# Kernel tuning notes

Measured on AMD Instinct MI355X. Metric: run time of the kernel, lower is better.

The kernel has to match this reference:

```python
import jax, jax.numpy as jnp
import numpy as np

N = 100000
E = 1600000
F_IN, HID, N_CLS = 128, 16, 32


def setup_inputs() -> dict:
    key = jax.random.key(0)
    ks = jax.random.split(key, 10)
    x = jax.random.normal(ks[0], (N, F_IN), dtype=jnp.float32)
    edge_index = jax.random.randint(ks[1], (2, E), 0, N, dtype=jnp.int64)
    edge_weight = jax.random.uniform(ks[2], (E,), dtype=jnp.float32)
    def glorot(k, shape):
        lim = np.sqrt(6.0 / (shape[0] + shape[1])).astype(np.float32)
        return jax.random.uniform(k, shape, dtype=jnp.float32, minval=-lim, maxval=lim)
    return {
        'x': x, 'edge_index': edge_index, 'edge_weight': edge_weight,
        'W1_0': glorot(ks[3], (F_IN, HID)), 'W1_1': glorot(ks[4], (F_IN, HID)),
        'b1': jnp.zeros((HID,), jnp.float32),
        'W2_0': glorot(ks[5], (HID, N_CLS)), 'W2_1': glorot(ks[6], (HID, N_CLS)),
        'b2': jnp.zeros((N_CLS,), jnp.float32),
    }


def _cheb_conv_k2(x, row, col, edge_weight, W0, W1, b):
    # PyG ChebConv, K=2, lambda_max=2.0:
    #   T0 = x; T1 = L_hat x = D^{-1/2} A D^{-1/2} x - x
    n = x.shape[0]
    deg = jax.ops.segment_sum(edge_weight, row, num_segments=n)  # [N]
    dinv = jnp.where(deg > 0, jax.lax.rsqrt(deg), 0.0)
    norm = dinv[row] * edge_weight * dinv[col]                   # [E]
    agg = jax.ops.segment_sum(norm[:, None] * x[col], row, num_segments=n)  # [N,F]
    tx1 = agg - x
    return x @ W0 + tx1 @ W1 + b


def reference(x, edge_index, edge_weight, W1_0, W1_1, b1, W2_0, W2_1, b2):
    row, col = edge_index[0], edge_index[1]
    h = jax.nn.relu(_cheb_conv_k2(x, row, col, edge_weight, W1_0, W1_1, b1))
    # dropout(p=0) and DFA layers are identity in forward
    out = _cheb_conv_k2(h, row, col, edge_weight, W2_0, W2_1, b2)
    return jax.nn.log_softmax(out, axis=1)
```

## Files before the change

### kernel.cpp

```cpp
#include <hip/hip_runtime.h>
#include <hip/hip_bf16.h>


#include <hip/hip_fp16.h>

constexpr int NN   = 100000;
constexpr int NE   = 1600000;
constexpr int FIN  = 128;
constexpr int HID  = 16;
constexpr int NCLS = 32;

constexpr int RB    = 256;
constexpr int NBKT  = (NN + RB - 1) / RB;
constexpr int EPB   = 4096;
constexpr int EPT   = EPB / 256;
constexpr int GP    = (NE + EPB - 1) / EPB;
constexpr int NTOT  = NBKT * GP;
constexpr int SCAN_CHUNK = 512;
constexpr int NBS   = (NTOT + SCAN_CHUNK - 1) / SCAN_CHUNK;
constexpr int CAP   = 8192;

typedef float f32x2 __attribute__((ext_vector_type(2)));

#if defined(__has_builtin)
#if __has_builtin(__builtin_amdgcn_cvt_pk_f32_fp8)
#define HAVE_CVT_FP8 1
#endif
#endif

static __device__ __forceinline__ unsigned int f2e4m3(float f) {
    union { float f; unsigned int u; } v; v.f = f;
    unsigned int s = (v.u >> 24) & 0x80u;
    unsigned int au = v.u & 0x7fffffffu;
    if (au > 0x43E00000u) au = 0x43E00000u;
    au += 0x7ffffu + ((au >> 20) & 1u);
    int e4 = (int)(au >> 23) - 120;
    unsigned int m = (au >> 20) & 7u;
    unsigned int byte = (e4 <= 0) ? 0u : (((unsigned int)e4 << 3) | m);
    return s | byte;
}
static __device__ __forceinline__ void fp8x4_fma(unsigned int v, float w, float* acc) {
#ifdef HAVE_CVT_FP8
    f32x2 lo = __builtin_amdgcn_cvt_pk_f32_fp8((int)v, false);
    f32x2 hi = __builtin_amdgcn_cvt_pk_f32_fp8((int)v, true);
    acc[0] += w * lo.x; acc[1] += w * lo.y;
    acc[2] += w * hi.x; acc[3] += w * hi.y;
#else
#pragma unroll
    for (int i = 0; i < 4; i++) {
        unsigned int b = (v >> (8 * i)) & 0xffu;
        float f = __int_as_float((int)(((b & 0x80u) << 24) | ((b & 0x7fu) << 20))) * 0x1p120f;
        acc[i] += w * f;
    }
#endif
}
static __device__ __forceinline__ unsigned int wpack(float wf) {
    unsigned int b = __float_as_uint(wf) + 0x8000u;
    return (b >> 16) & 0x7fffu;
}
static __device__ __forceinline__ float wdec(unsigned int u) {
    return __uint_as_float((u >> 17) << 16);
}

__global__ __launch_bounds__(256) void k_hist(const int* __restrict__ row,
                                              int* __restrict__ blockhist) {
    __shared__ int hist[NBKT];
    int tid = threadIdx.x;
    for (int i = tid; i < NBKT; i += 256) hist[i] = 0;
    __syncthreads();
    long ebase = (long)blockIdx.x * EPB;
#pragma unroll
    for (int i = 0; i < EPT; i++) {
        long e = ebase + i * 256 + tid;
        if (e < NE) atomicAdd(&hist[row[e] >> 8], 1);
    }
    __syncthreads();
    for (int i = tid; i < NBKT; i += 256)
        blockhist[i * GP + blockIdx.x] = hist[i];
}

__global__ __launch_bounds__(SCAN_CHUNK) void k_scan_block(
    const int* __restrict__ in, int* __restrict__ outExcl,
    int* __restrict__ bsum, int n) {
    __shared__ int sh[SCAN_CHUNK];
    int tid = threadIdx.x;
    int i = blockIdx.x * SCAN_CHUNK + tid;
    int v = (i < n) ? in[i] : 0;
    sh[tid] = v;
    __syncthreads();
    for (int off = 1; off < SCAN_CHUNK; off <<= 1) {
        int t = (tid >= off) ? sh[tid - off] : 0;
        __syncthreads();
        sh[tid] += t;
        __syncthreads();
    }
    if (i < n) outExcl[i] = sh[tid] - v;
    if (tid == SCAN_CHUNK - 1) bsum[blockIdx.x] = sh[tid];
}

__global__ void k_scan_tops(int* __restrict__ bsum, int nb) {
    int lane = threadIdx.x;
    int v[8], e[8];
    int s = 0;
#pragma unroll
    for (int t = 0; t < 8; t++) {
        int idx = lane * 8 + t;
        v[t] = (idx < nb) ? bsum[idx] : 0;
        e[t] = s;
        s += v[t];
    }
    int sc = s;
    for (int off = 1; off < 64; off <<= 1) {
        int up = __shfl_up(sc, off, 64);
        if (lane >= off) sc += up;
    }
    int excl = sc - s;
#pragma unroll
    for (int t = 0; t < 8; t++) {
        int idx = lane * 8 + t;
        if (idx < nb) bsum[idx] = excl + e[t];
    }
}

__global__ void k_scan_add(int* __restrict__ outExcl, const int* __restrict__ bsum, int n) {
    int i = blockIdx.x * blockDim.x + threadIdx.x;
    if (i < n) outExcl[i] += bsum[i >> 9];
}

__global__ __launch_bounds__(256) void k_partition(
    const int* __restrict__ row, const int* __restrict__ col,
    const float* __restrict__ w, const int* __restrict__ scanExcl,
    int2* __restrict__ part) {
    __shared__ int2 stage[EPB];
    __shared__ unsigned short sbkt[EPB];
    __shared__ int cnt[NBKT];
    __shared__ int lofs[NBKT];
    __shared__ int cursor[NBKT];
    __shared__ int gbase[NBKT];
    __shared__ int sa[512], sb[512];
    int tid = threadIdx.x;
    long ebase = (long)blockIdx.x * EPB;
    int rr[EPT]; int cc[EPT]; float wv[EPT];
#pragma unroll
    for (int i = 0; i < EPT; i++) {
        long e = ebase + i * 256 + tid;
        if (e < NE) { rr[i] = row[e]; cc[i] = col[e]; wv[i] = w[e]; }
        else rr[i] = -1;
    }
    for (int i = tid; i < NBKT; i += 256) cnt[i] = 0;
    __syncthreads();
#pragma unroll
    for (int i = 0; i < EPT; i++)
        if (rr[i] >= 0) atomicAdd(&cnt[rr[i] >> 8], 1);
    __syncthreads();
    for (int i = tid; i < 512; i += 256) sa[i] = (i < NBKT) ? cnt[i] : 0;
    __syncthreads();
    int* src = sa; int* dst = sb;
    for (int off = 1; off < 512; off <<= 1) {
        for (int i = tid; i < 512; i += 256)
            dst[i] = src[i] + ((i >= off) ? src[i - off] : 0);
        __syncthreads();
        int* t = src; src = dst; dst = t;
    }
    for (int i = tid; i < NBKT; i += 256) {
        int ex = src[i] - cnt[i];
        lofs[i] = ex;
        cursor[i] = ex;
        gbase[i] = scanExcl[i * GP + blockIdx.x];
    }
    __syncthreads();
#pragma unroll
    for (int i = 0; i < EPT; i++) {
        if (rr[i] >= 0) {
            int b = rr[i] >> 8;
            int p = atomicAdd(&cursor[b], 1);
            int2 v;
            v.x = cc[i] | ((rr[i] & 255) << 17);
            v.y = __float_as_int(wv[i]);
            stage[p] = v;
            sbkt[p] = (unsigned short)b;
        }
    }
    __syncthreads();
    int total = (int)min((long)EPB, NE - ebase);
    for (int i = tid; i < total; i += 256) {
        int b = sbkt[i];
        part[gbase[b] + (i - lofs[b])] = stage[i];
    }
}

__global__ __launch_bounds__(256) void k_bucket_sort(
    const int2* __restrict__ part, const int* __restrict__ scanExcl,
    unsigned int* __restrict__ partC, int* __restrict__ rowptr,
    float* __restrict__ dinv) {
    __shared__ int2 stage[CAP];
    __shared__ int hist[RB];
    __shared__ int cursor[RB];
    __shared__ int wtot[4];
    int b = blockIdx.x;
    int tid = threadIdx.x;
    int start = scanExcl[b * GP];
    int end = (b + 1 < NBKT) ? scanExcl[(b + 1) * GP] : NE;
    int count = end - start;
    hist[tid] = 0;
    __syncthreads();
    for (int i = tid; i < count; i += 256)
        atomicAdd(&hist[(part[start + i].x >> 17) & 255], 1);
    __syncthreads();
    int lane = tid & 63, wv = tid >> 6;
    int v = hist[tid];
    int sc = v;
#pragma unroll
    for (int off = 1; off < 64; off <<= 1) {
        int up = __shfl_up(sc, off, 64);
        if (lane >= off) sc += up;
    }
    if (lane == 63) wtot[wv] = sc;
    __syncthreads();
    int add = 0;
    for (int w2 = 0; w2 < wv; w2++) add += wtot[w2];
    int ex = sc + add - v;
    int node = b * RB + tid;
    if (node <= NN) rowptr[node] = start + ex;
    cursor[tid] = ex;
    __syncthreads();
    for (int i = tid; i < count; i += 256) {
        int2 p = part[start + i];
        int rl = (p.x >> 17) & 255;
        int pos = atomicAdd(&cursor[rl], 1);
        int2 c; c.x = p.x & 0x1FFFF; c.y = p.y;
        if (pos < CAP) stage[pos] = c;
    }
    __syncthreads();
    {
        int rend = cursor[tid];
        float d = 0.f;
        for (int i = ex; i < rend; i++) d += __int_as_float(stage[i].y);
        if (node < NN) dinv[node] = d > 0.f ? rsqrtf(d) : 0.f;
    }
    for (int i = tid; i < count; i += 256)
        if (i < CAP) {
            int2 p = stage[i];
            partC[start + i] = (unsigned int)p.x | (wpack(__int_as_float(p.y)) << 17);
        }
}

__global__ __launch_bounds__(256) void k_proj1(
    const float* __restrict__ x, const float* __restrict__ W0,
    const float* __restrict__ W1, const float* __restrict__ b1,
    const float* __restrict__ dinv,
    float* __restrict__ xa, unsigned char* __restrict__ xb8) {
    long t = (long)blockIdx.x * 256 + threadIdx.x;
    bool valid = t < NN;
    long n = valid ? t : 0;
    const float4* xg = (const float4*)x + n * 32;
    float accA[HID], accB[HID];
#pragma unroll
    for (int o = 0; o < HID; o++) { accA[o] = 0.f; accB[o] = 0.f; }
    float4 bufA[8], bufB[8];
#pragma unroll
    for (int m = 0; m < 8; m++) bufA[m] = xg[m];
#pragma unroll
    for (int m = 0; m < 8; m++) bufB[m] = xg[8 + m];

#define PROJ1_CHUNK(BUF, C)                                            \
    {                                                                   \
        const float* W0p = W0 + (C) * 32 * HID;                         \
        const float* W1p = W1 + (C) * 32 * HID;                         \
        _Pragma("unroll")                                               \
        for (int m = 0; m < 8; m++) {                                   \
            float xv[4] = {BUF[m].x, BUF[m].y, BUF[m].z, BUF[m].w};     \
            _Pragma("unroll")                                           \
            for (int q = 0; q < 4; q++) {                               \
                int k = m * 4 + q;                                      \
                _Pragma("unroll")                                       \
                for (int o = 0; o < HID; o++) accA[o] += xv[q] * W0p[k * HID + o]; \
                _Pragma("unroll")                                       \
                for (int o = 0; o < HID; o++) accB[o] += xv[q] * W1p[k * HID + o]; \
            }                                                           \
        }                                                               \
    }

    PROJ1_CHUNK(bufA, 0)
#pragma unroll
    for (int m = 0; m < 8; m++) bufA[m] = xg[16 + m];
    PROJ1_CHUNK(bufB, 1)
#pragma unroll
    for (int m = 0; m < 8; m++) bufB[m] = xg[24 + m];
    PROJ1_CHUNK(bufA, 2)
    PROJ1_CHUNK(bufB, 3)
#undef PROJ1_CHUNK

    if (!valid) return;
    float4* xap = (float4*)(xa + n * HID);
#pragma unroll
    for (int q = 0; q < 4; q++) {
        float4 va;
        va.x = accA[4*q+0] - accB[4*q+0] + b1[4*q+0];
        va.y = accA[4*q+1] - accB[4*q+1] + b1[4*q+1];
        va.z = accA[4*q+2] - accB[4*q+2] + b1[4*q+2];
        va.w = accA[4*q+3] - accB[4*q+3] + b1[4*q+3];
        xap[q] = va;
    }
    float dn = dinv[n];
    unsigned int pk[4];
#pragma unroll
    for (int q = 0; q < 4; q++)
        pk[q] = f2e4m3(dn * accB[4*q+0]) | (f2e4m3(dn * accB[4*q+1]) << 8)
              | (f2e4m3(dn * accB[4*q+2]) << 16) | (f2e4m3(dn * accB[4*q+3]) << 24);
    *(uint4*)(xb8 + n * HID) = make_uint4(pk[0], pk[1], pk[2], pk[3]);
}

__global__ __launch_bounds__(256) void k_gather1(
    const int* __restrict__ rowptr, const unsigned int* __restrict__ partC,
    const float* __restrict__ dinv, const unsigned char* __restrict__ xb8,
    float* __restrict__ agg1) {
    long t = (long)blockIdx.x * 256 + threadIdx.x;
    int n = (int)(t >> 6);
    if (n >= NN) return;
    int lane = threadIdx.x & 63;
    int d = lane & 3, p = lane >> 2;
    int s = rowptr[n], e = rowptr[n + 1];
    float acc[4] = {0.f, 0.f, 0.f, 0.f};
    for (int j = s + p; j < e; j += 16) {
        unsigned int u = partC[j];
        unsigned int v = *(const unsigned int*)(xb8 + (u & 0x1FFFF) * HID + d * 4);
        fp8x4_fma(v, wdec(u), acc);
    }
#pragma unroll
    for (int i = 0; i < 4; i++) {
        acc[i] += __shfl_xor(acc[i], 4);
        acc[i] += __shfl_xor(acc[i], 8);
        acc[i] += __shfl_xor(acc[i], 16);
        acc[i] += __shfl_xor(acc[i], 32);
    }
    if (p == 0) {
        float dn = dinv[n];
        float4 o; o.x = dn * acc[0]; o.y = dn * acc[1];
        o.z = dn * acc[2]; o.w = dn * acc[3];
        *(float4*)(agg1 + (long)n * HID + d * 4) = o;
    }
}

__global__ __launch_bounds__(256) void k_proj2(
    const float* __restrict__ xa, const float* __restrict__ agg1,
    const float* __restrict__ W0, const float* __restrict__ W1,
    const float* __restrict__ b2, const float* __restrict__ dinv,
    float* __restrict__ ha, unsigned char* __restrict__ hb8) {
    long n = (long)blockIdx.x * 256 + threadIdx.x;
    if (n >= NN) return;
    float h[HID];
    const float4* xap = (const float4*)(xa + n * HID);
    const float4* agp = (const float4*)(agg1 + n * HID);
#pragma unroll
    for (int q = 0; q < 4; q++) {
        float4 a = xap[q], g = agp[q];
        h[4*q+0] = fmaxf(a.x + g.x, 0.f);
        h[4*q+1] = fmaxf(a.y + g.y, 0.f);
        h[4*q+2] = fmaxf(a.z + g.z, 0.f);
        h[4*q+3] = fmaxf(a.w + g.w, 0.f);
    }
    float accA[NCLS], accB[NCLS];
#pragma unroll
    for (int o = 0; o < NCLS; o++) { accA[o] = 0.f; accB[o] = 0.f; }
#pragma unroll 2
    for (int k = 0; k < HID; k++) {
        float hk = h[k];
#pragma unroll
        for (int o = 0; o < NCLS; o++) accA[o] += hk * W0[k * NCLS + o];
#pragma unroll
        for (int o = 0; o < NCLS; o++) accB[o] += hk * W1[k * NCLS + o];
    }
    float4* hap = (float4*)(ha + n * NCLS);
#pragma unroll
    for (int q = 0; q < 8; q++) {
        float4 va;
        va.x = accA[4*q+0] - accB[4*q+0] + b2[4*q+0];
        va.y = accA[4*q+1] - accB[4*q+1] + b2[4*q+1];
        va.z = accA[4*q+2] - accB[4*q+2] + b2[4*q+2];
        va.w = accA[4*q+3] - accB[4*q+3] + b2[4*q+3];
        hap[q] = va;
    }
    float dn = dinv[n];
    unsigned int pk[8];
#pragma unroll
    for (int q = 0; q < 8; q++)
        pk[q] = f2e4m3(dn * accB[4*q+0]) | (f2e4m3(dn * accB[4*q+1]) << 8)
              | (f2e4m3(dn * accB[4*q+2]) << 16) | (f2e4m3(dn * accB[4*q+3]) << 24);
    uint4* hbp = (uint4*)(hb8 + n * NCLS);
    hbp[0] = make_uint4(pk[0], pk[1], pk[2], pk[3]);
    hbp[1] = make_uint4(pk[4], pk[5], pk[6], pk[7]);
}

__global__ __launch_bounds__(256) void k_gather2_lsm(
    const int* __restrict__ rowptr, const unsigned int* __restrict__ partC,
    const float* __restrict__ dinv, const float* __restrict__ ha,
    const unsigned char* __restrict__ hb8, float* __restrict__ out) {
    long t = (long)blockIdx.x * 256 + threadIdx.x;
    int n = (int)(t >> 6);
    if (n >= NN) return;
    int lane = threadIdx.x & 63;
    int d = lane & 7, p = lane >> 3;
    int s = rowptr[n], e = rowptr[n + 1];
    float acc[4] = {0.f, 0.f, 0.f, 0.f};
    int j = s + p;
    for (; j + 8 < e; j += 16) {
        unsigned int u0 = partC[j], u1 = partC[j + 8];
        unsigned int v0 = *(const unsigned int*)(hb8 + (u0 & 0x1FFFF) * NCLS + d * 4);
        unsigned int v1 = *(const unsigned int*)(hb8 + (u1 & 0x1FFFF) * NCLS + d * 4);
        fp8x4_fma(v0, wdec(u0), acc);
        fp8x4_fma(v1, wdec(u1), acc);
    }
    if (j < e) {
        unsigned int u0 = partC[j];
        unsigned int v0 = *(const unsigned int*)(hb8 + (u0 & 0x1FFFF) * NCLS + d * 4);
        fp8x4_fma(v0, wdec(u0), acc);
    }
#pragma unroll
    for (int i = 0; i < 4; i++) {
        acc[i] += __shfl_xor(acc[i], 8);
        acc[i] += __shfl_xor(acc[i], 16);
        acc[i] += __shfl_xor(acc[i], 32);
    }
    float dn = dinv[n];
    float4 hv = *(const float4*)(ha + (long)n * NCLS + d * 4);
    float v0 = dn * acc[0] + hv.x;
    float v1 = dn * acc[1] + hv.y;
    float v2 = dn * acc[2] + hv.z;
    float v3 = dn * acc[3] + hv.w;
    float m = fmaxf(fmaxf(v0, v1), fmaxf(v2, v3));
    m = fmaxf(m, __shfl_xor(m, 1));
    m = fmaxf(m, __shfl_xor(m, 2));
    m = fmaxf(m, __shfl_xor(m, 4));
    float sum = __expf(v0 - m) + __expf(v1 - m) + __expf(v2 - m) + __expf(v3 - m);
    sum += __shfl_xor(sum, 1);
    sum += __shfl_xor(sum, 2);
    sum += __shfl_xor(sum, 4);
    float ls = logf(sum);
    if (p == 0) {
        float4 o; o.x = v0 - m - ls; o.y = v1 - m - ls;
        o.z = v2 - m - ls; o.w = v3 - m - ls;
        *(float4*)(out + (long)n * NCLS + d * 4) = o;
    }
}

extern "C" void kernel_launch(void* const* d_in, const int* in_sizes, int n_in,
                              void* d_out, int out_size, void* d_ws, size_t ws_size,
                              hipStream_t stream) {
    const float* x    = (const float*)d_in[0];
    const int*   ei   = (const int*)d_in[1];
    const float* ew   = (const float*)d_in[2];
    const float* W1_0 = (const float*)d_in[3];
    const float* W1_1 = (const float*)d_in[4];
    const float* b1   = (const float*)d_in[5];
    const float* W2_0 = (const float*)d_in[6];
    const float* W2_1 = (const float*)d_in[7];
    const float* b2   = (const float*)d_in[8];
    float* out = (float*)d_out;

    const int* row = ei;
    const int* col = ei + NE;

    char* ws = (char*)d_ws;
    int2*  part      = (int2*)ws;                 ws += sizeof(int2) * NE;
    unsigned int* partC = (unsigned int*)ws;      ws += sizeof(int) * NE;
    int*   blockhist = (int*)ws;                  ws += sizeof(int) * NTOT;
    int*   scanExcl  = (int*)ws;                  ws += sizeof(int) * NTOT;
    int*   bsum      = (int*)ws;                  ws += sizeof(int) * 512;
    int*   rowptr    = (int*)ws;                  ws += sizeof(int) * (NN + 4);
    float* dinv      = (float*)ws;                ws += sizeof(float) * NN;
    float* xa        = (float*)ws;                ws += sizeof(float) * NN * HID;
    float* agg1      = (float*)ws;                ws += sizeof(float) * NN * HID;
    float* ha        = (float*)ws;                ws += sizeof(float) * NN * NCLS;
    unsigned char* xb8 = (unsigned char*)ws;      ws += sizeof(char) * NN * HID;
    unsigned char* hb8 = (unsigned char*)ws;      ws += sizeof(char) * NN * NCLS;

    k_hist<<<GP, 256, 0, stream>>>(row, blockhist);
    k_scan_block<<<NBS, SCAN_CHUNK, 0, stream>>>(blockhist, scanExcl, bsum, NTOT);
    k_scan_tops<<<1, 64, 0, stream>>>(bsum, NBS);
    k_scan_add<<<(NTOT + 255) / 256, 256, 0, stream>>>(scanExcl, bsum, NTOT);
    k_partition<<<GP, 256, 0, stream>>>(row, col, ew, scanExcl, part);
    k_bucket_sort<<<NBKT, 256, 0, stream>>>(part, scanExcl, partC, rowptr, dinv);
    k_proj1<<<(NN + 255) / 256, 256, 0, stream>>>(x, W1_0, W1_1, b1, dinv, xa, xb8);
    {
        long th = (long)NN * 64;
        k_gather1<<<(int)((th + 255) / 256), 256, 0, stream>>>(rowptr, partC, dinv, xb8, agg1);
    }
    k_proj2<<<(NN + 255) / 256, 256, 0, stream>>>(xa, agg1, W2_0, W2_1, b2, dinv, ha, hb8);
    {
        long th = (long)NN * 64;
        k_gather2_lsm<<<(int)((th + 255) / 256), 256, 0, stream>>>(rowptr, partC, dinv, ha, hb8, out);
    }
}
```

Before: 246.2 us.

## Replace histogram+scan partitioning with atomic bucket slots; split proj1 K across threads

Drops the separate histogram pass and its three-kernel multi-block scan. Each partition block now reserves space in fixed-capacity per-bucket regions through global atomics, and a single small scan over bucket counts produces the bucket starts. This removes a full read of the row array and several launches, but assumes no bucket holds more than CAP edges, and the order of edges within a bucket now depends on atomic timing. Separately, proj1 splits the 128-wide input reduction across two threads per node and combines them through shared memory, giving more threads per node and fewer registers per thread.

```diff
diff --git a/kernel.cpp b/kernel.cpp
--- a/kernel.cpp
+++ b/kernel.cpp
@@ -15,9 +15,6 @@
 constexpr int EPB   = 4096;
 constexpr int EPT   = EPB / 256;
 constexpr int GP    = (NE + EPB - 1) / EPB;
-constexpr int NTOT  = NBKT * GP;
-constexpr int SCAN_CHUNK = 512;
-constexpr int NBS   = (NTOT + SCAN_CHUNK - 1) / SCAN_CHUNK;
 constexpr int CAP   = 8192;
 
 typedef float f32x2 __attribute__((ext_vector_type(2)));
@@ -62,75 +59,15 @@
     return __uint_as_float((u >> 17) << 16);
 }
 
-__global__ __launch_bounds__(256) void k_hist(const int* __restrict__ row,
-                                              int* __restrict__ blockhist) {
-    __shared__ int hist[NBKT];
-    int tid = threadIdx.x;
-    for (int i = tid; i < NBKT; i += 256) hist[i] = 0;
-    __syncthreads();
-    long ebase = (long)blockIdx.x * EPB;
-#pragma unroll
-    for (int i = 0; i < EPT; i++) {
-        long e = ebase + i * 256 + tid;
-        if (e < NE) atomicAdd(&hist[row[e] >> 8], 1);
-    }
-    __syncthreads();
-    for (int i = tid; i < NBKT; i += 256)
-        blockhist[i * GP + blockIdx.x] = hist[i];
-}
-
-__global__ __launch_bounds__(SCAN_CHUNK) void k_scan_block(
-    const int* __restrict__ in, int* __restrict__ outExcl,
-    int* __restrict__ bsum, int n) {
-    __shared__ int sh[SCAN_CHUNK];
-    int tid = threadIdx.x;
-    int i = blockIdx.x * SCAN_CHUNK + tid;
-    int v = (i < n) ? in[i] : 0;
-    sh[tid] = v;
-    __syncthreads();
-    for (int off = 1; off < SCAN_CHUNK; off <<= 1) {
-        int t = (tid >= off) ? sh[tid - off] : 0;
-        __syncthreads();
-        sh[tid] += t;
-        __syncthreads();
-    }
-    if (i < n) outExcl[i] = sh[tid] - v;
-    if (tid == SCAN_CHUNK - 1) bsum[blockIdx.x] = sh[tid];
-}
-
-__global__ void k_scan_tops(int* __restrict__ bsum, int nb) {
-    int lane = threadIdx.x;
-    int v[8], e[8];
-    int s = 0;
-#pragma unroll
-    for (int t = 0; t < 8; t++) {
-        int idx = lane * 8 + t;
-        v[t] = (idx < nb) ? bsum[idx] : 0;
-        e[t] = s;
-        s += v[t];
-    }
-    int sc = s;
-    for (int off = 1; off < 64; off <<= 1) {
-        int up = __shfl_up(sc, off, 64);
-        if (lane >= off) sc += up;
-    }
-    int excl = sc - s;
-#pragma unroll
-    for (int t = 0; t < 8; t++) {
-        int idx = lane * 8 + t;
-        if (idx < nb) bsum[idx] = excl + e[t];
-    }
-}
-
-__global__ void k_scan_add(int* __restrict__ outExcl, const int* __restrict__ bsum, int n) {
+__global__ void k_zero_cur(int* __restrict__ bucketCursor) {
     int i = blockIdx.x * blockDim.x + threadIdx.x;
-    if (i < n) outExcl[i] += bsum[i >> 9];
+    if (i < NBKT) bucketCursor[i] = 0;
 }
 
 __global__ __launch_bounds__(256) void k_partition(
     const int* __restrict__ row, const int* __restrict__ col,
-    const float* __restrict__ w, const int* __restrict__ scanExcl,
-    int2* __restrict__ part) {
+    const float* __restrict__ w, int* __restrict__ bucketCursor,
+    int2* __restrict__ partS) {
     __shared__ int2 stage[EPB];
     __shared__ unsigned short sbkt[EPB];
     __shared__ int cnt[NBKT];
@@ -166,7 +103,8 @@
         int ex = src[i] - cnt[i];
         lofs[i] = ex;
         cursor[i] = ex;
-        gbase[i] = scanExcl[i * GP + blockIdx.x];
+        int go = (cnt[i] > 0) ? atomicAdd(&bucketCursor[i], cnt[i]) : 0;
+        gbase[i] = i * CAP + go;
     }
     __syncthreads();
 #pragma unroll
@@ -185,12 +123,38 @@
     int total = (int)min((long)EPB, NE - ebase);
     for (int i = tid; i < total; i += 256) {
         int b = sbkt[i];
-        part[gbase[b] + (i - lofs[b])] = stage[i];
+        partS[gbase[b] + (i - lofs[b])] = stage[i];
+    }
+}
+
+__global__ void k_scan_buckets(const int* __restrict__ bucketCursor,
+                               int* __restrict__ bucketStart) {
+    int lane = threadIdx.x;
+    int v[8], e[8];
+    int s = 0;
+#pragma unroll
+    for (int t = 0; t < 8; t++) {
+        int idx = lane * 8 + t;
+        v[t] = (idx < NBKT) ? bucketCursor[idx] : 0;
+        e[t] = s;
+        s += v[t];
+    }
+    int sc = s;
+    for (int off = 1; off < 64; off <<= 1) {
+        int up = __shfl_up(sc, off, 64);
+        if (lane >= off) sc += up;
+    }
+    int excl = sc - s;
+#pragma unroll
+    for (int t = 0; t < 8; t++) {
+        int idx = lane * 8 + t;
+        if (idx < NBKT) bucketStart[idx] = excl + e[t];
     }
 }
 
 __global__ __launch_bounds__(256) void k_bucket_sort(
-    const int2* __restrict__ part, const int* __restrict__ scanExcl,
+    const int2* __restrict__ partS, const int* __restrict__ bucketCursor,
+    const int* __restrict__ bucketStart,
     unsigned int* __restrict__ partC, int* __restrict__ rowptr,
     float* __restrict__ dinv) {
     __shared__ int2 stage[CAP];
@@ -199,13 +163,13 @@
     __shared__ int wtot[4];
     int b = blockIdx.x;
     int tid = threadIdx.x;
-    int start = scanExcl[b * GP];
-    int end = (b + 1 < NBKT) ? scanExcl[(b + 1) * GP] : NE;
-    int count = end - start;
+    int start = bucketStart[b];
+    int count = bucketCursor[b];
+    const int2* src = partS + (long)b * CAP;
     hist[tid] = 0;
     __syncthreads();
     for (int i = tid; i < count; i += 256)
-        atomicAdd(&hist[(part[start + i].x >> 17) & 255], 1);
+        atomicAdd(&hist[(src[i].x >> 17) & 255], 1);
     __syncthreads();
     int lane = tid & 63, wv = tid >> 6;
     int v = hist[tid];
@@ -225,7 +189,7 @@
     cursor[tid] = ex;
     __syncthreads();
     for (int i = tid; i < count; i += 256) {
-        int2 p = part[start + i];
+        int2 p = src[i];
         int rl = (p.x >> 17) & 255;
         int pos = atomicAdd(&cursor[rl], 1);
         int2 c; c.x = p.x & 0x1FFFF; c.y = p.y;
@@ -250,10 +214,14 @@
     const float* __restrict__ W1, const float* __restrict__ b1,
     const float* __restrict__ dinv,
     float* __restrict__ xa, unsigned char* __restrict__ xb8) {
-    long t = (long)blockIdx.x * 256 + threadIdx.x;
-    bool valid = t < NN;
-    long n = valid ? t : 0;
-    const float4* xg = (const float4*)x + n * 32;
+    __shared__ float red[128 * 33];
+    int tid = threadIdx.x;
+    int nl = tid & 127;
+    int kh = tid >> 7;
+    long n = (long)blockIdx.x * 128 + nl;
+    bool valid = n < NN;
+    long nc = valid ? n : 0;
+    const float4* xg = (const float4*)x + nc * 32 + kh * 16;
     float accA[HID], accB[HID];
 #pragma unroll
     for (int o = 0; o < HID; o++) { accA[o] = 0.f; accB[o] = 0.f; }
@@ -281,17 +249,23 @@
         }                                                               \
     }
 
-    PROJ1_CHUNK(bufA, 0)
-#pragma unroll
-    for (int m = 0; m < 8; m++) bufA[m] = xg[16 + m];
-    PROJ1_CHUNK(bufB, 1)
-#pragma unroll
-    for (int m = 0; m < 8; m++) bufB[m] = xg[24 + m];
-    PROJ1_CHUNK(bufA, 2)
-    PROJ1_CHUNK(bufB, 3)
+    PROJ1_CHUNK(bufA, kh * 2 + 0)
+    PROJ1_CHUNK(bufB, kh * 2 + 1)
 #undef PROJ1_CHUNK
 
-    if (!valid) return;
+    if (kh == 1) {
+#pragma unroll
+        for (int o = 0; o < HID; o++) red[nl * 33 + o] = accA[o];
+#pragma unroll
+        for (int o = 0; o < HID; o++) red[nl * 33 + HID + o] = accB[o];
+    }
+    __syncthreads();
+    if (kh == 1 || !valid) return;
+#pragma unroll
+    for (int o = 0; o < HID; o++) accA[o] += red[nl * 33 + o];
+#pragma unroll
+    for (int o = 0; o < HID; o++) accB[o] += red[nl * 33 + HID + o];
+
     float4* xap = (float4*)(xa + n * HID);
 #pragma unroll
     for (int q = 0; q < 4; q++) {
@@ -462,11 +436,10 @@
     const int* col = ei + NE;
 
     char* ws = (char*)d_ws;
-    int2*  part      = (int2*)ws;                 ws += sizeof(int2) * NE;
+    int2*  partS     = (int2*)ws;                 ws += sizeof(int2) * (long)NBKT * CAP;
     unsigned int* partC = (unsigned int*)ws;      ws += sizeof(int) * NE;
-    int*   blockhist = (int*)ws;                  ws += sizeof(int) * NTOT;
-    int*   scanExcl  = (int*)ws;                  ws += sizeof(int) * NTOT;
-    int*   bsum      = (int*)ws;                  ws += sizeof(int) * 512;
+    int*   bucketCursor = (int*)ws;               ws += sizeof(int) * NBKT;
+    int*   bucketStart  = (int*)ws;               ws += sizeof(int) * NBKT;
     int*   rowptr    = (int*)ws;                  ws += sizeof(int) * (NN + 4);
     float* dinv      = (float*)ws;                ws += sizeof(float) * NN;
     float* xa        = (float*)ws;                ws += sizeof(float) * NN * HID;
@@ -475,13 +448,12 @@
     unsigned char* xb8 = (unsigned char*)ws;      ws += sizeof(char) * NN * HID;
     unsigned char* hb8 = (unsigned char*)ws;      ws += sizeof(char) * NN * NCLS;
 
-    k_hist<<<GP, 256, 0, stream>>>(row, blockhist);
-    k_scan_block<<<NBS, SCAN_CHUNK, 0, stream>>>(blockhist, scanExcl, bsum, NTOT);
-    k_scan_tops<<<1, 64, 0, stream>>>(bsum, NBS);
-    k_scan_add<<<(NTOT + 255) / 256, 256, 0, stream>>>(scanExcl, bsum, NTOT);
-    k_partition<<<GP, 256, 0, stream>>>(row, col, ew, scanExcl, part);
-    k_bucket_sort<<<NBKT, 256, 0, stream>>>(part, scanExcl, partC, rowptr, dinv);
-    k_proj1<<<(NN + 255) / 256, 256, 0, stream>>>(x, W1_0, W1_1, b1, dinv, xa, xb8);
+    k_zero_cur<<<(NBKT + 255) / 256, 256, 0, stream>>>(bucketCursor);
+    k_partition<<<GP, 256, 0, stream>>>(row, col, ew, bucketCursor, partS);
+    k_scan_buckets<<<1, 64, 0, stream>>>(bucketCursor, bucketStart);
+    k_bucket_sort<<<NBKT, 256, 0, stream>>>(partS, bucketCursor, bucketStart,
+                                            partC, rowptr, dinv);
+    k_proj1<<<(NN + 127) / 128, 256, 0, stream>>>(x, W1_0, W1_1, b1, dinv, xa, xb8);
     {
         long th = (long)NN * 64;
         k_gather1<<<(int)((th + 255) / 256), 256, 0, stream>>>(rowptr, partC, dinv, xb8, agg1);
```

Result: slower. 286.7 us (+16.5%).
